# Performance work log

Hardware: AMD Instinct MI355X
Metric: run time of the kernel (lower is better)

Reference implementation:

```python
import jax, jax.numpy as jnp
import numpy as np

NUM_HEADS = 8
ROPE_BASE = 10000.0

def rotate_half(x):
    x1, x2 = jnp.split(x, 2, axis=-1)
    return jnp.concatenate((-x2, x1), axis=-1)

def rope_cos_sin(seq_len, head_dim, dtype):
    inv_freq = 1.0 / (ROPE_BASE ** (jnp.arange(0, head_dim, 2, dtype=jnp.float32) / head_dim))
    t = jnp.arange(seq_len, dtype=jnp.float32)
    freqs = t[:, None] * inv_freq[None, :]            # [N, D/2]
    emb = jnp.concatenate((freqs, freqs), axis=-1)    # [N, D]
    cos = jnp.cos(emb)[None, None].astype(dtype)      # [1,1,N,D]
    sin = jnp.sin(emb)[None, None].astype(dtype)
    return cos, sin

def setup_inputs() -> dict:
    key = jax.random.key(0)
    k1, k2, k3 = jax.random.split(key, 3)
    B, N, C = 4, 2048, 512
    x = jax.random.normal(k1, (B, N, C), dtype=jnp.float32)
    w_qkv = jax.random.normal(k2, (C, 3 * C), dtype=jnp.float32) * (C ** -0.5)
    w_proj = jax.random.normal(k3, (C, C), dtype=jnp.float32) * (C ** -0.5)
    b_proj = jnp.zeros((C,), dtype=jnp.float32)
    return {"x": x, "w_qkv": w_qkv, "w_proj": w_proj, "b_proj": b_proj}

def reference(x, w_qkv, w_proj, b_proj):
    B, N, C = x.shape
    H = NUM_HEADS
    D = C // H
    scale = D ** -0.5
    qkv = (x @ w_qkv).reshape(B, N, 3, H, D).transpose(2, 0, 3, 1, 4)  # [3,B,H,N,D]
    q, k, v = qkv[0], qkv[1], qkv[2]
    cos, sin = rope_cos_sin(N, D, x.dtype)
    q = q * cos + rotate_half(q) * sin
    k = k * cos + rotate_half(k) * sin
    attn = jax.nn.softmax(jnp.einsum('bhnd,bhmd->bhnm', q, k) * scale, axis=-1)  # [B,H,N,N]
    out = jnp.einsum('bhnm,bhmd->bhnd', attn, v)      # [B,H,N,D]
    out = out.transpose(0, 2, 1, 3).reshape(B, N, C)
    out = out @ w_proj + b_proj
    return out, attn
```

## Files before the change

kernel.cpp:

```cpp
#include <hip/hip_runtime.h>
#include <math.h>


#define OFF_K 4194304
#define OFF_V 8388608

typedef float nf4 __attribute__((ext_vector_type(4)));

#define SWZ(row, col) (((((col) >> 2) ^ (((row) >> 2) & 7)) << 2) | ((col) & 3))

__global__ __launch_bounds__(256) void gemm_qkv_kernel(
    const float* __restrict__ x, const float* __restrict__ w,
    float* __restrict__ qb, float* __restrict__ kb, float* __restrict__ vb)
{
    __shared__ float As[8][132];
    __shared__ float Bs[8][132];
    const int tid  = threadIdx.x;
    const int row0 = blockIdx.x * 128;
    const int col0 = blockIdx.y * 128;
    const int tx = tid & 15, ty = tid >> 4;

    float acc[8][8];
    #pragma unroll
    for (int i = 0; i < 8; ++i)
        #pragma unroll
        for (int j = 0; j < 8; ++j) acc[i][j] = 0.0f;

    const int ar  = tid >> 1;
    const int ah  = (tid & 1) * 4;
    const int bkr = tid >> 5;
    const int bc  = (tid & 31) * 4;

    for (int k0 = 0; k0 < 512; k0 += 8) {
        float4 a4 = *(const float4*)(x + (size_t)(row0 + ar) * 512 + k0 + ah);
        float4 b4 = *(const float4*)(w + (size_t)(k0 + bkr) * 1536 + col0 + bc);
        __syncthreads();
        As[ah + 0][ar] = a4.x; As[ah + 1][ar] = a4.y;
        As[ah + 2][ar] = a4.z; As[ah + 3][ar] = a4.w;
        *(float4*)&Bs[bkr][bc] = b4;
        __syncthreads();
        #pragma unroll
        for (int kk = 0; kk < 8; ++kk) {
            float a[8], b[8];
            *(float4*)&a[0] = *(const float4*)&As[kk][ty * 8];
            *(float4*)&a[4] = *(const float4*)&As[kk][ty * 8 + 4];
            *(float4*)&b[0] = *(const float4*)&Bs[kk][tx * 8];
            *(float4*)&b[4] = *(const float4*)&Bs[kk][tx * 8 + 4];
            #pragma unroll
            for (int i = 0; i < 8; ++i)
                #pragma unroll
                for (int j = 0; j < 8; ++j)
                    acc[i][j] = fmaf(a[i], b[j], acc[i][j]);
        }
    }

    #pragma unroll
    for (int i = 0; i < 8; ++i) {
        int r  = row0 + ty * 8 + i;
        int b_ = r >> 11;
        int n  = r & 2047;
        #pragma unroll
        for (int j0 = 0; j0 < 8; j0 += 4) {
            int c     = col0 + tx * 8 + j0;
            int which = c >> 9;
            int h     = (c >> 6) & 7;
            int d     = c & 63;
            float* base = (which == 0) ? qb : ((which == 1) ? kb : vb);
            float* dst  = base + (((size_t)(b_ * 8 + h) * 2048 + n) * 64 + d);
            *(float4*)dst = make_float4(acc[i][j0], acc[i][j0 + 1],
                                        acc[i][j0 + 2], acc[i][j0 + 3]);
        }
    }
}

__global__ void rope_kernel(float* __restrict__ qb, float* __restrict__ kb)
{
    int idx = blockIdx.x * 256 + threadIdx.x;
    if (idx >= 4 * 8 * 2048 * 32) return;
    int i  = idx & 31;
    int n  = (idx >> 5) & 2047;
    int bh = idx >> 16;

    double invf = pow(10000.0, -(double)(2 * i) / 64.0);
    double ang  = (double)n * invf;
    float c = (float)cos(ang);
    float s = (float)sin(ang);

    size_t base = ((size_t)bh * 2048 + n) * 64;
    float q0 = qb[base + i], q1 = qb[base + i + 32];
    qb[base + i]      = q0 * c - q1 * s;
    qb[base + i + 32] = q1 * c + q0 * s;
    float k0 = kb[base + i], k1 = kb[base + i + 32];
    kb[base + i]      = k0 * c - k1 * s;
    kb[base + i + 32] = k1 * c + k0 * s;
}

__global__ __launch_bounds__(256) void attn_scores_pv_kernel(
    const float* __restrict__ qb, const float* __restrict__ kb,
    const float* __restrict__ vb, float* __restrict__ attn,
    float* __restrict__ out_pre)
{
    __shared__ float smem[19072];
    float (*Qs)[132] = (float (*)[132])smem;
    float (*Ks)[132] = (float (*)[132])(smem + 8448);
    float (*Ps)[132] = (float (*)[132])smem;
    float (*Vs)[68]  = (float (*)[68])(smem + 8448);
    float (*mt)[16]  = (float (*)[16])(smem + 16896);
    float* l_lds     = smem + 18944;

    const int tid = threadIdx.x;
    const int bh  = blockIdx.x;
    const int n0  = blockIdx.y * 128;
    const int tx = tid & 15, ty = tid >> 4;

    const float* qbase = qb + ((size_t)bh * 2048 + n0) * 64;
    const float* kbase = kb + (size_t)bh * 2048 * 64;
    const float* vbase = vb + (size_t)bh * 2048 * 64;
    float* attn_base = attn + ((size_t)bh * 2048 + n0) * 2048;

    #pragma unroll
    for (int it = 0; it < 8; ++it) {
        int r = ty + it * 16;
        int d = tx * 4;
        float4 v4 = *(const float4*)(qbase + (size_t)r * 64 + d);
        int pc = SWZ(d, r);
        Qs[d + 0][pc] = v4.x * 0.125f; Qs[d + 1][pc] = v4.y * 0.125f;
        Qs[d + 2][pc] = v4.z * 0.125f; Qs[d + 3][pc] = v4.w * 0.125f;
    }
    float m[8], l[8];
    #pragma unroll
    for (int i = 0; i < 8; ++i) { m[i] = -3.0e38f; l[i] = 0.0f; }
    __syncthreads();

    for (int m0 = 0; m0 < 2048; m0 += 128) {
        float4 kv[8];
        #pragma unroll
        for (int it = 0; it < 8; ++it) {
            int c = ty + it * 16;
            kv[it] = *(const float4*)(kbase + (size_t)(m0 + c) * 64 + tx * 4);
        }
        __syncthreads();
        #pragma unroll
        for (int it = 0; it < 8; ++it) {
            int c = ty + it * 16;
            int d = tx * 4;
            int pc = SWZ(d, c);
            Ks[d + 0][pc] = kv[it].x; Ks[d + 1][pc] = kv[it].y;
            Ks[d + 2][pc] = kv[it].z; Ks[d + 3][pc] = kv[it].w;
        }
        __syncthreads();

        float acc[8][8];
        #pragma unroll
        for (int i = 0; i < 8; ++i)
            #pragma unroll
            for (int j = 0; j < 8; ++j) acc[i][j] = 0.0f;

        #pragma unroll 4
        for (int d = 0; d < 64; ++d) {
            const int sk = (d >> 2) & 7;
            float a[8], b[8];
            *(float4*)&a[0] = *(const float4*)&Qs[d][((ty * 2 + 0) ^ sk) << 2];
            *(float4*)&a[4] = *(const float4*)&Qs[d][((ty * 2 + 1) ^ sk) << 2];
            *(float4*)&b[0] = *(const float4*)&Ks[d][((tx * 2 + 0) ^ sk) << 2];
            *(float4*)&b[4] = *(const float4*)&Ks[d][((tx * 2 + 1) ^ sk) << 2];
            #pragma unroll
            for (int i = 0; i < 8; ++i)
                #pragma unroll
                for (int j = 0; j < 8; ++j)
                    acc[i][j] = fmaf(a[i], b[j], acc[i][j]);
        }

        #pragma unroll
        for (int i = 0; i < 8; ++i) {
            float mx = acc[i][0];
            #pragma unroll
            for (int j = 1; j < 8; ++j) mx = fmaxf(mx, acc[i][j]);
            mx = fmaxf(mx, __shfl_xor(mx, 1));
            mx = fmaxf(mx, __shfl_xor(mx, 2));
            mx = fmaxf(mx, __shfl_xor(mx, 4));
            mx = fmaxf(mx, __shfl_xor(mx, 8));
            float mn = fmaxf(m[i], mx);
            l[i] *= __expf(m[i] - mn);
            m[i]  = mn;
            float s = 0.0f;
            #pragma unroll
            for (int j = 0; j < 8; ++j) {
                acc[i][j] = __expf(acc[i][j] - mn);
                s += acc[i][j];
            }
            s += __shfl_xor(s, 1);
            s += __shfl_xor(s, 2);
            s += __shfl_xor(s, 4);
            s += __shfl_xor(s, 8);
            l[i] += s;
        }

        #pragma unroll
        for (int i = 0; i < 8; ++i) {
            int r = ty * 8 + i;
            float* drow = attn_base + (size_t)r * 2048 + m0 + tx * 8;
            *(float4*)drow       = make_float4(acc[i][0], acc[i][1], acc[i][2], acc[i][3]);
            *(float4*)(drow + 4) = make_float4(acc[i][4], acc[i][5], acc[i][6], acc[i][7]);
        }
        if (tx == 0) {
            int t = m0 >> 7;
            #pragma unroll
            for (int i = 0; i < 8; ++i) mt[ty * 8 + i][t] = m[i];
        }
    }
    if (tx == 0) {
        #pragma unroll
        for (int i = 0; i < 8; ++i) l_lds[ty * 8 + i] = l[i];
    }
    __syncthreads();

    {
        int r  = tid >> 1;
        int c0 = (tid & 1) * 8;
        float v[8];
        #pragma unroll
        for (int j = 0; j < 8; ++j) v[j] = mt[r][c0 + j];
        float mf = mt[r][15];
        float lv = l_lds[r];
        __syncthreads();
        #pragma unroll
        for (int j = 0; j < 8; ++j) mt[r][c0 + j] = __expf(v[j] - mf) / lv;
    }
    __syncthreads();

    float accO[8][4];
    #pragma unroll
    for (int i = 0; i < 8; ++i)
        #pragma unroll
        for (int j = 0; j < 4; ++j) accO[i][j] = 0.0f;

    for (int s0 = 0; s0 < 2048; s0 += 64) {
        const int t = s0 >> 7;
        float4 vv[4];
        #pragma unroll
        for (int it = 0; it < 4; ++it)
            vv[it] = *(const float4*)(vbase + (size_t)(s0 + ty + it * 16) * 64 + tx * 4);

        float4 pp[8];
        #pragma unroll
        for (int it = 0; it < 8; ++it) {
            int r = ty + it * 16;
            float c = mt[r][t];
            float* prow = attn_base + (size_t)r * 2048 + s0 + tx * 4;
            float4 s4 = *(const float4*)prow;
            s4.x *= c; s4.y *= c; s4.z *= c; s4.w *= c;
            pp[it] = s4;
            nf4 nt = { s4.x, s4.y, s4.z, s4.w };
            __builtin_nontemporal_store(nt, (nf4*)prow);
        }

        __syncthreads();
        #pragma unroll
        for (int it = 0; it < 4; ++it)
            *(float4*)&Vs[ty + it * 16][tx * 4] = vv[it];
        #pragma unroll
        for (int it = 0; it < 8; ++it) {
            int r = ty + it * 16;
            int mcol = tx * 4;
            int pc = SWZ(mcol, r);
            Ps[mcol + 0][pc] = pp[it].x; Ps[mcol + 1][pc] = pp[it].y;
            Ps[mcol + 2][pc] = pp[it].z; Ps[mcol + 3][pc] = pp[it].w;
        }
        __syncthreads();

        #pragma unroll 4
        for (int kk = 0; kk < 64; ++kk) {
            const int sk = (kk >> 2) & 7;
            float a[8], b[4];
            *(float4*)&a[0] = *(const float4*)&Ps[kk][((ty * 2 + 0) ^ sk) << 2];
            *(float4*)&a[4] = *(const float4*)&Ps[kk][((ty * 2 + 1) ^ sk) << 2];
            *(float4*)&b[0] = *(const float4*)&Vs[kk][tx * 4];
            #pragma unroll
            for (int i = 0; i < 8; ++i)
                #pragma unroll
                for (int j = 0; j < 4; ++j)
                    accO[i][j] = fmaf(a[i], b[j], accO[i][j]);
        }
    }

    #pragma unroll
    for (int i = 0; i < 8; ++i) {
        float* dst = out_pre + ((size_t)bh * 2048 + n0 + ty * 8 + i) * 64 + tx * 4;
        *(float4*)dst = make_float4(accO[i][0], accO[i][1], accO[i][2], accO[i][3]);
    }
}

__global__ __launch_bounds__(256) void proj_kernel(
    const float* __restrict__ a, const float* __restrict__ w,
    const float* __restrict__ bias, float* __restrict__ out)
{
    __shared__ float As[8][132];
    __shared__ float Bs[8][132];
    const int tid  = threadIdx.x;
    const int row0 = blockIdx.x * 128;
    const int col0 = blockIdx.y * 128;
    const int tx = tid & 15, ty = tid >> 4;

    float acc[8][8];
    #pragma unroll
    for (int i = 0; i < 8; ++i)
        #pragma unroll
        for (int j = 0; j < 8; ++j) acc[i][j] = 0.0f;

    const int ar  = tid >> 1;
    const int ah  = (tid & 1) * 4;
    const int bkr = tid >> 5;
    const int bc  = (tid & 31) * 4;

    const int r_  = row0 + ar;
    const int b_  = r_ >> 11;
    const int n_  = r_ & 2047;

    for (int k0 = 0; k0 < 512; k0 += 8) {
        const int kk_ = k0 + ah;
        const int h_  = kk_ >> 6;
        const int d_  = kk_ & 63;
        float4 a4 = *(const float4*)(a + (((size_t)(b_ * 8 + h_) * 2048 + n_) * 64 + d_));
        float4 b4 = *(const float4*)(w + (size_t)(k0 + bkr) * 512 + col0 + bc);
        __syncthreads();
        As[ah + 0][ar] = a4.x; As[ah + 1][ar] = a4.y;
        As[ah + 2][ar] = a4.z; As[ah + 3][ar] = a4.w;
        *(float4*)&Bs[bkr][bc] = b4;
        __syncthreads();
        #pragma unroll
        for (int kk = 0; kk < 8; ++kk) {
            float av[8], bv[8];
            *(float4*)&av[0] = *(const float4*)&As[kk][ty * 8];
            *(float4*)&av[4] = *(const float4*)&As[kk][ty * 8 + 4];
            *(float4*)&bv[0] = *(const float4*)&Bs[kk][tx * 8];
            *(float4*)&bv[4] = *(const float4*)&Bs[kk][tx * 8 + 4];
            #pragma unroll
            for (int i = 0; i < 8; ++i)
                #pragma unroll
                for (int j = 0; j < 8; ++j)
                    acc[i][j] = fmaf(av[i], bv[j], acc[i][j]);
        }
    }

    float bj[8];
    #pragma unroll
    for (int j = 0; j < 8; ++j) bj[j] = bias[col0 + tx * 8 + j];

    #pragma unroll
    for (int i = 0; i < 8; ++i) {
        int r = row0 + ty * 8 + i;
        float* dst = out + (size_t)r * 512 + col0 + tx * 8;
        *(float4*)dst       = make_float4(acc[i][0] + bj[0], acc[i][1] + bj[1],
                                          acc[i][2] + bj[2], acc[i][3] + bj[3]);
        *(float4*)(dst + 4) = make_float4(acc[i][4] + bj[4], acc[i][5] + bj[5],
                                          acc[i][6] + bj[6], acc[i][7] + bj[7]);
    }
}

extern "C" void kernel_launch(void* const* d_in, const int* in_sizes, int n_in,
                              void* d_out, int out_size, void* d_ws, size_t ws_size,
                              hipStream_t stream)
{
    const float* x      = (const float*)d_in[0];
    const float* w_qkv  = (const float*)d_in[1];
    const float* w_proj = (const float*)d_in[2];
    const float* b_proj = (const float*)d_in[3];

    float* out  = (float*)d_out;
    float* attn = (float*)d_out + 4194304;

    float* ws = (float*)d_ws;
    float* q = ws;
    float* k = ws + OFF_K;
    float* v = ws + OFF_V;
    float* out_pre = ws;

    gemm_qkv_kernel<<<dim3(64, 12), 256, 0, stream>>>(x, w_qkv, q, k, v);
    rope_kernel<<<8192, 256, 0, stream>>>(q, k);
    attn_scores_pv_kernel<<<dim3(32, 16), 256, 0, stream>>>(q, k, v, attn, out_pre);
    proj_kernel<<<dim3(64, 4), 256, 0, stream>>>(out_pre, w_proj, b_proj, out);
}
```

Baseline: 1.372 ms.

## Recompute QK^T in second pass to write attention probabilities once

Pass 1 now only accumulates the running row max and sum. It no longer writes unnormalized exponentials to the attention output. Pass 2 reloads K and V tiles, recomputes the scores, normalizes them with the final max and 1/l, stores the probabilities with non-temporal stores, and feeds them through LDS into the PV product. This drops one full write and one full read of the large attention matrix in exchange for computing QK^T twice, with a reworked shared-memory layout.

```diff
diff --git a/kernel.cpp b/kernel.cpp
--- a/kernel.cpp
+++ b/kernel.cpp
@@ -95,18 +95,17 @@
     kb[base + i + 32] = k1 * c + k0 * s;
 }
 
-__global__ __launch_bounds__(256) void attn_scores_pv_kernel(
+__global__ __launch_bounds__(256) void attn_fused_kernel(
     const float* __restrict__ qb, const float* __restrict__ kb,
     const float* __restrict__ vb, float* __restrict__ attn,
     float* __restrict__ out_pre)
 {
-    __shared__ float smem[19072];
-    float (*Qs)[132] = (float (*)[132])smem;
-    float (*Ks)[132] = (float (*)[132])(smem + 8448);
-    float (*Ps)[132] = (float (*)[132])smem;
-    float (*Vs)[68]  = (float (*)[68])(smem + 8448);
-    float (*mt)[16]  = (float (*)[16])(smem + 16896);
-    float* l_lds     = smem + 18944;
+    __shared__ float smem[20480];
+    float (*Qs)[128]  = (float (*)[128])smem;
+    float (*Ks)[128]  = (float (*)[128])(smem + 8192);
+    float (*Ks64)[64] = (float (*)[64])(smem + 8192);
+    float (*Ps)[128]  = (float (*)[128])(smem + 8192);
+    float (*Vs)[64]   = (float (*)[64])(smem + 16384);
 
     const int tid = threadIdx.x;
     const int bh  = blockIdx.x;
@@ -185,97 +184,93 @@
             m[i]  = mn;
             float s = 0.0f;
             #pragma unroll
-            for (int j = 0; j < 8; ++j) {
-                acc[i][j] = __expf(acc[i][j] - mn);
-                s += acc[i][j];
-            }
+            for (int j = 0; j < 8; ++j) s += __expf(acc[i][j] - mn);
             s += __shfl_xor(s, 1);
             s += __shfl_xor(s, 2);
             s += __shfl_xor(s, 4);
             s += __shfl_xor(s, 8);
             l[i] += s;
         }
+    }
+
+    float linv[8];
+    #pragma unroll
+    for (int i = 0; i < 8; ++i) linv[i] = 1.0f / l[i];
+
+    float accO[8][4];
+    #pragma unroll
+    for (int i = 0; i < 8; ++i)
+        #pragma unroll
+        for (int j = 0; j < 4; ++j) accO[i][j] = 0.0f;
+
+    for (int s0 = 0; s0 < 2048; s0 += 64) {
+        float4 kk4[4], vv4[4];
+        #pragma unroll
+        for (int it = 0; it < 4; ++it) {
+            int row = s0 + ty + it * 16;
+            kk4[it] = *(const float4*)(kbase + (size_t)row * 64 + tx * 4);
+            vv4[it] = *(const float4*)(vbase + (size_t)row * 64 + tx * 4);
+        }
+        __syncthreads();
+        #pragma unroll
+        for (int it = 0; it < 4; ++it) {
+            int c = ty + it * 16;
+            int d = tx * 4;
+            int pc = SWZ(d, c);
+            Ks64[d + 0][pc] = kk4[it].x; Ks64[d + 1][pc] = kk4[it].y;
+            Ks64[d + 2][pc] = kk4[it].z; Ks64[d + 3][pc] = kk4[it].w;
+            *(float4*)&Vs[c][tx * 4] = vv4[it];
+        }
+        __syncthreads();
+
+        float acc2[8][4];
+        #pragma unroll
+        for (int i = 0; i < 8; ++i)
+            #pragma unroll
+            for (int j = 0; j < 4; ++j) acc2[i][j] = 0.0f;
+
+        #pragma unroll 4
+        for (int d = 0; d < 64; ++d) {
+            const int sk = (d >> 2) & 7;
+            float a[8], b[4];
+            *(float4*)&a[0] = *(const float4*)&Qs[d][((ty * 2 + 0) ^ sk) << 2];
+            *(float4*)&a[4] = *(const float4*)&Qs[d][((ty * 2 + 1) ^ sk) << 2];
+            *(float4*)&b[0] = *(const float4*)&Ks64[d][(tx ^ sk) << 2];
+            #pragma unroll
+            for (int i = 0; i < 8; ++i)
+                #pragma unroll
+                for (int j = 0; j < 4; ++j)
+                    acc2[i][j] = fmaf(a[i], b[j], acc2[i][j]);
+        }
 
         #pragma unroll
         for (int i = 0; i < 8; ++i) {
-            int r = ty * 8 + i;
-            float* drow = attn_base + (size_t)r * 2048 + m0 + tx * 8;
-            *(float4*)drow       = make_float4(acc[i][0], acc[i][1], acc[i][2], acc[i][3]);
-            *(float4*)(drow + 4) = make_float4(acc[i][4], acc[i][5], acc[i][6], acc[i][7]);
-        }
-        if (tx == 0) {
-            int t = m0 >> 7;
-            #pragma unroll
-            for (int i = 0; i < 8; ++i) mt[ty * 8 + i][t] = m[i];
-        }
-    }
-    if (tx == 0) {
-        #pragma unroll
-        for (int i = 0; i < 8; ++i) l_lds[ty * 8 + i] = l[i];
-    }
-    __syncthreads();
-
-    {
-        int r  = tid >> 1;
-        int c0 = (tid & 1) * 8;
-        float v[8];
-        #pragma unroll
-        for (int j = 0; j < 8; ++j) v[j] = mt[r][c0 + j];
-        float mf = mt[r][15];
-        float lv = l_lds[r];
-        __syncthreads();
-        #pragma unroll
-        for (int j = 0; j < 8; ++j) mt[r][c0 + j] = __expf(v[j] - mf) / lv;
-    }
-    __syncthreads();
-
-    float accO[8][4];
-    #pragma unroll
-    for (int i = 0; i < 8; ++i)
-        #pragma unroll
-        for (int j = 0; j < 4; ++j) accO[i][j] = 0.0f;
-
-    for (int s0 = 0; s0 < 2048; s0 += 64) {
-        const int t = s0 >> 7;
-        float4 vv[4];
-        #pragma unroll
-        for (int it = 0; it < 4; ++it)
-            vv[it] = *(const float4*)(vbase + (size_t)(s0 + ty + it * 16) * 64 + tx * 4);
-
-        float4 pp[8];
-        #pragma unroll
-        for (int it = 0; it < 8; ++it) {
-            int r = ty + it * 16;
-            float c = mt[r][t];
-            float* prow = attn_base + (size_t)r * 2048 + s0 + tx * 4;
-            float4 s4 = *(const float4*)prow;
-            s4.x *= c; s4.y *= c; s4.z *= c; s4.w *= c;
-            pp[it] = s4;
-            nf4 nt = { s4.x, s4.y, s4.z, s4.w };
+            #pragma unroll
+            for (int j = 0; j < 4; ++j)
+                acc2[i][j] = __expf(acc2[i][j] - m[i]) * linv[i];
+            nf4 nt = { acc2[i][0], acc2[i][1], acc2[i][2], acc2[i][3] };
+            float* prow = attn_base + (size_t)(ty * 8 + i) * 2048 + s0 + tx * 4;
             __builtin_nontemporal_store(nt, (nf4*)prow);
         }
 
         __syncthreads();
         #pragma unroll
-        for (int it = 0; it < 4; ++it)
-            *(float4*)&Vs[ty + it * 16][tx * 4] = vv[it];
-        #pragma unroll
-        for (int it = 0; it < 8; ++it) {
-            int r = ty + it * 16;
-            int mcol = tx * 4;
-            int pc = SWZ(mcol, r);
-            Ps[mcol + 0][pc] = pp[it].x; Ps[mcol + 1][pc] = pp[it].y;
-            Ps[mcol + 2][pc] = pp[it].z; Ps[mcol + 3][pc] = pp[it].w;
+        for (int jj = 0; jj < 4; ++jj) {
+            #pragma unroll
+            for (int i = 0; i < 8; ++i) {
+                int pc = ((((ty * 2 + (i >> 2)) ^ (tx & 7)) << 2) | (i & 3));
+                Ps[tx * 4 + jj][pc] = acc2[i][jj];
+            }
         }
         __syncthreads();
 
         #pragma unroll 4
-        for (int kk = 0; kk < 64; ++kk) {
-            const int sk = (kk >> 2) & 7;
+        for (int kkp = 0; kkp < 64; ++kkp) {
+            const int skp = (kkp >> 2) & 7;
             float a[8], b[4];
-            *(float4*)&a[0] = *(const float4*)&Ps[kk][((ty * 2 + 0) ^ sk) << 2];
-            *(float4*)&a[4] = *(const float4*)&Ps[kk][((ty * 2 + 1) ^ sk) << 2];
-            *(float4*)&b[0] = *(const float4*)&Vs[kk][tx * 4];
+            *(float4*)&a[0] = *(const float4*)&Ps[kkp][((ty * 2 + 0) ^ skp) << 2];
+            *(float4*)&a[4] = *(const float4*)&Ps[kkp][((ty * 2 + 1) ^ skp) << 2];
+            *(float4*)&b[0] = *(const float4*)&Vs[kkp][tx * 4];
             #pragma unroll
             for (int i = 0; i < 8; ++i)
                 #pragma unroll
@@ -378,6 +373,6 @@
 
     gemm_qkv_kernel<<<dim3(64, 12), 256, 0, stream>>>(x, w_qkv, q, k, v);
     rope_kernel<<<8192, 256, 0, stream>>>(q, k);
-    attn_scores_pv_kernel<<<dim3(32, 16), 256, 0, stream>>>(q, k, v, attn, out_pre);
+    attn_fused_kernel<<<dim3(32, 16), 256, 0, stream>>>(q, k, v, attn, out_pre);
     proj_kernel<<<dim3(64, 4), 256, 0, stream>>>(out_pre, w_proj, b_proj, out);
 }
```

Result: slower. 1.407 ms (+2.6%).
